# Optimization experiments

Hardware: AMD Instinct MI355X
Metric: run time of the kernel (lower is better)

## Reference

```python
import jax, jax.numpy as jnp
import numpy as np
import math

L_MAX = 4  # len(type): spherical harmonics for l = 0 .. L_MAX-1
B, N = 8, 256


def _spharm_all(X):
    """Complex orthonormal spherical harmonics Y_l^m for all l<L_MAX, m in [-l,l],
    evaluated at every point X[..., :3]. Returns real view [..., L_MAX**2, 2]
    (last dim = (real, imag)), components ordered (l, m) with m ascending."""
    x, y, z = X[..., 0], X[..., 1], X[..., 2]
    r = jnp.sqrt(x * x + y * y + z * z)
    ct = z / r                                   # cos(theta)
    st = jnp.sqrt(jnp.clip(1.0 - ct * ct, 0.0, 1.0))  # sin(theta) >= 0
    phi = jnp.arctan2(y, x)

    # Associated Legendre P_l^m(ct) with Condon-Shortley phase, via standard recurrences.
    P = {(0, 0): jnp.ones_like(ct)}
    for m in range(L_MAX):
        if m > 0:
            P[(m, m)] = (-(2 * m - 1)) * st * P[(m - 1, m - 1)]
        if m + 1 < L_MAX:
            P[(m + 1, m)] = (2 * m + 1) * ct * P[(m, m)]
        for l in range(m + 2, L_MAX):
            P[(l, m)] = ((2 * l - 1) * ct * P[(l - 1, m)] - (l + m - 1) * P[(l - 2, m)]) / (l - m)

    comps = []
    for l in range(L_MAX):
        for m in range(-l, l + 1):
            am = abs(m)
            nlm = math.sqrt((2 * l + 1) / (4.0 * math.pi)
                            * math.factorial(l - am) / math.factorial(l + am))
            base = jnp.float32(nlm) * P[(l, am)]
            re = base * jnp.cos(am * phi)
            im = base * jnp.sin(am * phi)
            if m < 0:  # Y_l^{-m} = (-1)^m conj(Y_l^m)
                sgn = (-1.0) ** am
                re, im = sgn * re, -sgn * im
            comps.append(jnp.stack([re, im], axis=-1))  # [B,N,N,2]
    return jnp.stack(comps, axis=-2)  # [B, N, N, L_MAX**2, 2]


def setup_inputs() -> dict:
    key = jax.random.key(0)
    X = jax.random.normal(key, (B, N, N, 3), dtype=jnp.float32)
    return {"X": X}


def reference(X):
    # Vectorized replacement for the quadruple Python loop over (l, b, i, j)
    # calling SO3part.spharm per point. Output packs all l-parts (2l+1 each,
    # sum = L_MAX**2 = 16) along axis -2, complex as (real, imag) on axis -1.
    return _spharm_all(X)
```

## Files before the change

kernel.cpp:

```cpp
#include <hip/hip_runtime.h>


constexpr int PTS_PER_BLOCK = 256;

__global__ __launch_bounds__(256) void spharm16_kernel(const float* __restrict__ X,
                                                       float4* __restrict__ out4,
                                                       int npts) {
    __shared__ float4 lds[PTS_PER_BLOCK * 8];

    const int t = threadIdx.x;
    const int p = blockIdx.x * PTS_PER_BLOCK + t;
    const int pc = (p < npts) ? p : (npts - 1);

    const float x = X[3 * pc + 0];
    const float y = X[3 * pc + 1];
    const float z = X[3 * pc + 2];

    const float r2   = x * x + y * y + z * z;
    const float rinv = rsqrtf(r2);
    const float ct   = z * rinv;
    const float ct2  = ct * ct;
    const float st2  = fmaxf(1.0f - ct2, 0.0f);
    const float st   = sqrtf(st2);

    const float rho2 = x * x + y * y;
    const float pinv = rsqrtf(rho2);
    const bool  okp  = rho2 > 0.0f;
    const float c1   = okp ? x * pinv : 1.0f;
    const float s1   = okp ? y * pinv : 0.0f;
    const float c2   = c1 * c1 - s1 * s1;
    const float s2   = 2.0f * c1 * s1;
    const float c3   = c2 * c1 - s2 * s1;
    const float s3   = s2 * c1 + c2 * s1;

    const float S1  = 0.34549414947133547f * st;
    const float B10 = 0.48860251190291992f * ct;
    const float B20 = 0.63078313050504031f * (1.5f * ct2 - 0.5f);
    const float T21 = 0.77254840404637910f * ct * st;
    const float B22 = 0.38627420202318955f * st2;
    const float B30 = 0.74635266518023080f * ct * (2.5f * ct2 - 1.5f);
    const float B31 = 0.32318018411248776f * st * (1.0f - 5.0f * ct2);
    const float B32 = 1.02198547643188850f * ct * st2;
    const float T33 = 0.41722382363278404f * st2 * st;

    const float S1c1 = S1 * c1,  S1s1 = S1 * s1;
    const float T21c1 = T21 * c1, T21s1 = T21 * s1;
    const float B22c2 = B22 * c2, B22s2 = B22 * s2;
    const float B31c1 = B31 * c1, B31s1 = B31 * s1;
    const float B32c2 = B32 * c2, B32s2 = B32 * s2;
    const float T33c3 = T33 * c3, T33s3 = T33 * s3;

    const int wb = t * 8;
    const int sw = t & 7;
    lds[wb + (0 ^ sw)] = make_float4(0.28209479177387814f, 0.0f, S1c1, -S1s1);
    lds[wb + (1 ^ sw)] = make_float4(B10, 0.0f, -S1c1, -S1s1);
    lds[wb + (2 ^ sw)] = make_float4(B22c2, -B22s2, T21c1, -T21s1);
    lds[wb + (3 ^ sw)] = make_float4(B20, 0.0f, -T21c1, -T21s1);
    lds[wb + (4 ^ sw)] = make_float4(B22c2, B22s2, T33c3, -T33s3);
    lds[wb + (5 ^ sw)] = make_float4(B32c2, -B32s2, -B31c1, B31s1);
    lds[wb + (6 ^ sw)] = make_float4(B30, 0.0f, B31c1, B31s1);
    lds[wb + (7 ^ sw)] = make_float4(B32c2, B32s2, -T33c3, -T33s3);

    __syncthreads();

    const int base4 = blockIdx.x * (PTS_PER_BLOCK * 8);
    const int nf4   = npts * 8;
    if (base4 + PTS_PER_BLOCK * 8 <= nf4) {
#pragma unroll
        for (int j = 0; j < 8; ++j) {
            const int i4 = j * 256 + t;
            const int pl = i4 >> 3;
            const int c4 = i4 & 7;
            out4[base4 + i4] = lds[pl * 8 + (c4 ^ (pl & 7))];
        }
    } else {
#pragma unroll
        for (int j = 0; j < 8; ++j) {
            const int i4 = j * 256 + t;
            const int g4 = base4 + i4;
            if (g4 < nf4) {
                const int pl = i4 >> 3;
                const int c4 = i4 & 7;
                out4[g4] = lds[pl * 8 + (c4 ^ (pl & 7))];
            }
        }
    }
}

extern "C" void kernel_launch(void* const* d_in, const int* in_sizes, int n_in,
                              void* d_out, int out_size, void* d_ws, size_t ws_size,
                              hipStream_t stream) {
    const float* X = (const float*)d_in[0];
    float4* out4 = (float4*)d_out;
    const int npts = in_sizes[0] / 3;
    const int blocks = (npts + PTS_PER_BLOCK - 1) / PTS_PER_BLOCK;
    spharm16_kernel<<<blocks, PTS_PER_BLOCK, 0, stream>>>(X, out4, npts);
}
```

Before: 76.21 us.

## Assign eight threads per point and drop LDS staging for output

Each thread now owns one float4 of the output and recomputes the full harmonic set for its point, picking its slice with a select tree. This removes the shared-memory transpose and block barrier and gives eight times more threads for latency hiding. In exchange, the per-point arithmetic and input loads are repeated eight times.

```diff
diff --git a/kernel.cpp b/kernel.cpp
--- a/kernel.cpp
+++ b/kernel.cpp
@@ -1,20 +1,23 @@
 #include <hip/hip_runtime.h>
 
 
-constexpr int PTS_PER_BLOCK = 256;
+constexpr int TPB = 256;
+
+__device__ __forceinline__ float4 sel4(bool c, const float4& a, const float4& b) {
+    return make_float4(c ? a.x : b.x, c ? a.y : b.y, c ? a.z : b.z, c ? a.w : b.w);
+}
 
 __global__ __launch_bounds__(256) void spharm16_kernel(const float* __restrict__ X,
                                                        float4* __restrict__ out4,
-                                                       int npts) {
-    __shared__ float4 lds[PTS_PER_BLOCK * 8];
+                                                       int nf4) {
+    const int gt = blockIdx.x * TPB + threadIdx.x;
+    if (gt >= nf4) return;
+    const int p = gt >> 3;
+    const int q = gt & 7;
 
-    const int t = threadIdx.x;
-    const int p = blockIdx.x * PTS_PER_BLOCK + t;
-    const int pc = (p < npts) ? p : (npts - 1);
-
-    const float x = X[3 * pc + 0];
-    const float y = X[3 * pc + 1];
-    const float z = X[3 * pc + 2];
+    const float x = X[3 * p + 0];
+    const float y = X[3 * p + 1];
+    const float z = X[3 * p + 2];
 
     const float r2   = x * x + y * y + z * z;
     const float rinv = rsqrtf(r2);
@@ -43,48 +46,34 @@
     const float B32 = 1.02198547643188850f * ct * st2;
     const float T33 = 0.41722382363278404f * st2 * st;
 
-    const float S1c1 = S1 * c1,  S1s1 = S1 * s1;
+    const float S1c1  = S1  * c1, S1s1  = S1  * s1;
     const float T21c1 = T21 * c1, T21s1 = T21 * s1;
     const float B22c2 = B22 * c2, B22s2 = B22 * s2;
     const float B31c1 = B31 * c1, B31s1 = B31 * s1;
     const float B32c2 = B32 * c2, B32s2 = B32 * s2;
     const float T33c3 = T33 * c3, T33s3 = T33 * s3;
 
-    const int wb = t * 8;
-    const int sw = t & 7;
-    lds[wb + (0 ^ sw)] = make_float4(0.28209479177387814f, 0.0f, S1c1, -S1s1);
-    lds[wb + (1 ^ sw)] = make_float4(B10, 0.0f, -S1c1, -S1s1);
-    lds[wb + (2 ^ sw)] = make_float4(B22c2, -B22s2, T21c1, -T21s1);
-    lds[wb + (3 ^ sw)] = make_float4(B20, 0.0f, -T21c1, -T21s1);
-    lds[wb + (4 ^ sw)] = make_float4(B22c2, B22s2, T33c3, -T33s3);
-    lds[wb + (5 ^ sw)] = make_float4(B32c2, -B32s2, -B31c1, B31s1);
-    lds[wb + (6 ^ sw)] = make_float4(B30, 0.0f, B31c1, B31s1);
-    lds[wb + (7 ^ sw)] = make_float4(B32c2, B32s2, -T33c3, -T33s3);
+    const float4 q0 = make_float4(0.28209479177387814f, 0.0f,  S1c1, -S1s1);
+    const float4 q1 = make_float4(B10,    0.0f,  -S1c1,  -S1s1);
+    const float4 q2 = make_float4(B22c2, -B22s2,  T21c1, -T21s1);
+    const float4 q3 = make_float4(B20,    0.0f,  -T21c1, -T21s1);
+    const float4 q4 = make_float4(B22c2,  B22s2,  T33c3, -T33s3);
+    const float4 q5 = make_float4(B32c2, -B32s2, -B31c1,  B31s1);
+    const float4 q6 = make_float4(B30,    0.0f,   B31c1,  B31s1);
+    const float4 q7 = make_float4(B32c2,  B32s2, -T33c3, -T33s3);
 
-    __syncthreads();
+    const bool b0 = (q & 1) != 0;
+    const bool b1 = (q & 2) != 0;
+    const bool b2 = (q & 4) != 0;
+    const float4 m01 = sel4(b0, q1, q0);
+    const float4 m23 = sel4(b0, q3, q2);
+    const float4 m45 = sel4(b0, q5, q4);
+    const float4 m67 = sel4(b0, q7, q6);
+    const float4 n0  = sel4(b1, m23, m01);
+    const float4 n1  = sel4(b1, m67, m45);
+    const float4 res = sel4(b2, n1, n0);
 
-    const int base4 = blockIdx.x * (PTS_PER_BLOCK * 8);
-    const int nf4   = npts * 8;
-    if (base4 + PTS_PER_BLOCK * 8 <= nf4) {
-#pragma unroll
-        for (int j = 0; j < 8; ++j) {
-            const int i4 = j * 256 + t;
-            const int pl = i4 >> 3;
-            const int c4 = i4 & 7;
-            out4[base4 + i4] = lds[pl * 8 + (c4 ^ (pl & 7))];
-        }
-    } else {
-#pragma unroll
-        for (int j = 0; j < 8; ++j) {
-            const int i4 = j * 256 + t;
-            const int g4 = base4 + i4;
-            if (g4 < nf4) {
-                const int pl = i4 >> 3;
-                const int c4 = i4 & 7;
-                out4[g4] = lds[pl * 8 + (c4 ^ (pl & 7))];
-            }
-        }
-    }
+    out4[gt] = res;
 }
 
 extern "C" void kernel_launch(void* const* d_in, const int* in_sizes, int n_in,
@@ -93,6 +82,7 @@
     const float* X = (const float*)d_in[0];
     float4* out4 = (float4*)d_out;
     const int npts = in_sizes[0] / 3;
-    const int blocks = (npts + PTS_PER_BLOCK - 1) / PTS_PER_BLOCK;
-    spharm16_kernel<<<blocks, PTS_PER_BLOCK, 0, stream>>>(X, out4, npts);
+    const int nf4  = npts * 8;
+    const int blocks = (nf4 + TPB - 1) / TPB;
+    spharm16_kernel<<<blocks, TPB, 0, stream>>>(X, out4, nf4);
 }
```

After: 77.29 us (median of 2 runs). No clear change (+1.4%).
